# Kernel optimization log

Hardware: AMD Instinct MI355X
Metric: run time of the kernel (lower is better)

## Reference

```python
import jax, jax.numpy as jnp
import numpy as np

B, T, C, UNITS = 64, 1000, 320, 320


def _lstm_scan(x_tbc, m_tb, W, U, b):
    """Masked LSTM over leading time axis.
    x_tbc: [T,B,C], m_tb: [T,B] bool. Keras gate order i,f,c(g),o.
    Masked steps carry (h,c) through unchanged and emit the carried h,
    matching Keras masking semantics. Returns (ys [T,B,U], h_T [B,U]).
    """
    units = U.shape[0]
    h0 = jnp.zeros((x_tbc.shape[1], units), x_tbc.dtype)

    def step(carry, inp):
        h, c = carry
        xt, mt = inp
        z = xt @ W + h @ U + b                      # [B, 4U]
        i, f, g, o = jnp.split(z, 4, axis=-1)
        i = jax.nn.sigmoid(i)
        f = jax.nn.sigmoid(f)
        g = jnp.tanh(g)
        o = jax.nn.sigmoid(o)
        c_new = f * c + i * g
        h_new = o * jnp.tanh(c_new)
        mt = mt[:, None]
        h = jnp.where(mt, h_new, h)
        c = jnp.where(mt, c_new, c)
        return (h, c), h

    (hT, cT), ys = jax.lax.scan(step, (h0, h0), (x_tbc, m_tb))
    return ys, hT


def setup_inputs() -> dict:
    key = jax.random.key(0)
    ks = jax.random.split(key, 8)
    inputs = jax.random.normal(ks[0], (B, T, C), dtype=jnp.float32)
    # padding mask: variable sequence lengths in [T//2, T]
    seq_len = jax.random.randint(ks[1], (B,), T // 2, T + 1)
    mask = (jnp.arange(T)[None, :] < seq_len[:, None])  # [B, T] bool
    s_in = 1.0 / np.sqrt(C)
    s_rec = 1.0 / np.sqrt(UNITS)
    W_fwd = jax.random.normal(ks[2], (C, 4 * UNITS), jnp.float32) * s_in
    U_fwd = jax.random.normal(ks[3], (UNITS, 4 * UNITS), jnp.float32) * s_rec
    b_fwd = jnp.zeros((4 * UNITS,), jnp.float32).at[UNITS:2 * UNITS].set(1.0)  # unit forget bias
    W_bwd = jax.random.normal(ks[4], (C, 4 * UNITS), jnp.float32) * s_in
    U_bwd = jax.random.normal(ks[5], (UNITS, 4 * UNITS), jnp.float32) * s_rec
    b_bwd = jnp.zeros((4 * UNITS,), jnp.float32).at[UNITS:2 * UNITS].set(1.0)
    return {"inputs": inputs, "mask": mask, "W_fwd": W_fwd, "U_fwd": U_fwd,
            "b_fwd": b_fwd, "W_bwd": W_bwd, "U_bwd": U_bwd, "b_bwd": b_bwd}


def reference(inputs, mask, W_fwd, U_fwd, b_fwd, W_bwd, U_bwd, b_bwd):
    x = jnp.transpose(inputs, (1, 0, 2))   # [T,B,C]
    m = jnp.transpose(mask, (1, 0))        # [T,B]
    # forward direction
    ys_f, h_f = _lstm_scan(x, m, W_fwd, U_fwd, b_fwd)
    # backward direction: go_backwards reverses time; Bidirectional flips output back
    ys_b, h_b = _lstm_scan(x[::-1], m[::-1], W_bwd, U_bwd, b_bwd)
    ys_b = ys_b[::-1]
    sequence_output = jnp.transpose(jnp.concatenate([ys_f, ys_b], axis=-1), (1, 0, 2))  # [B,T,2U]
    state_output = jnp.concatenate([h_f, h_b], axis=-1)  # [B,2U]
    return sequence_output, state_output
```

## Files before the change

### kernel.cpp

```cpp
#include <hip/hip_runtime.h>
#include <hip/hip_bf16.h>
#include <stdint.h>


#define Bx 64
#define Tx 1000
#define Cx 320
#define NSLICE 20
#define UPW 16
#define SENT 0xFFFFFFFFFFFFFFFFull

typedef __attribute__((ext_vector_type(8))) short short8;
typedef __attribute__((ext_vector_type(4))) short short4v;
typedef __attribute__((ext_vector_type(4))) float f32x4;

__device__ inline unsigned short f2bf(float f) {
  unsigned x = __builtin_bit_cast(unsigned, f);
  x += 0x7fffu + ((x >> 16) & 1u);
  return (unsigned short)(x >> 16);
}
__device__ inline float bf2f(unsigned short u) {
  unsigned x = ((unsigned)u) << 16;
  return __builtin_bit_cast(float, x);
}

#define OFF_MB   0ull
#define OFF_HB   16384ull
#define OFF_XB   0ull
#define OFF_WT   40960000ull
#define OFF_BP   42598400ull
#define OFF_ZX   42608640ull

__global__ __launch_bounds__(256) void k_prep_x(const float* __restrict__ X,
                                                unsigned short* __restrict__ Xb) {
  int i4 = blockIdx.x * 256 + threadIdx.x;
  if (i4 >= Bx * Tx * Cx / 4) return;
  int idx = i4 * 4;
  int b = idx / (Tx * Cx);
  int rem = idx - b * (Tx * Cx);
  int t = rem / Cx;
  int c = rem - t * Cx;
  float4 v = *(const float4*)(X + idx);
  short4v o;
  o[0] = (short)f2bf(v.x); o[1] = (short)f2bf(v.y);
  o[2] = (short)f2bf(v.z); o[3] = (short)f2bf(v.w);
  *(short4v*)(Xb + (size_t)(t * Bx + b) * Cx + c) = o;
}

__global__ __launch_bounds__(256) void k_prep_w(const float* __restrict__ Wf,
                                                const float* __restrict__ Wb,
                                                const float* __restrict__ bfv,
                                                const float* __restrict__ bbv,
                                                unsigned short* __restrict__ Wt,
                                                float* __restrict__ biasp) {
  int gid = blockIdx.x * 256 + threadIdx.x;
  if (gid < 2 * 1280 * 320) {
    int dir = gid / (1280 * 320);
    int rem = gid - dir * 1280 * 320;
    int n = rem / 320;
    int k = rem - n * 320;
    const float* W = dir ? Wb : Wf;
    Wt[gid] = f2bf(W[k * 1280 + n]);
  }
  if (gid < 2 * 1280) {
    int dir = gid / 1280, n = gid - dir * 1280;
    const float* bsrc = dir ? bbv : bfv;
    biasp[gid] = bsrc[n];
  }
}

__global__ __launch_bounds__(256) void k_prep_mask(const void* __restrict__ maskp,
                                                   unsigned long long* __restrict__ mask2) {
  int t = blockIdx.x * 256 + threadIdx.x;
  if (t >= Tx) return;
  const unsigned* mw = (const unsigned*)maskp;
  const bool mbyte = (mw[0] == 0x01010101u);
  unsigned long long wv = 0ull;
  if (mbyte) {
    const unsigned char* m8 = (const unsigned char*)maskp;
#pragma unroll 8
    for (int b = 0; b < Bx; b++)
      wv |= (unsigned long long)(m8[b * Tx + t] & 1) << b;
  } else {
    const int* m32 = (const int*)maskp;
#pragma unroll 8
    for (int b = 0; b < Bx; b++)
      wv |= (unsigned long long)(m32[b * Tx + t] & 1) << b;
  }
  mask2[t] = wv;
}

__global__ __launch_bounds__(256) void k_gemm(const unsigned short* __restrict__ A,
                                              const unsigned short* __restrict__ Bt,
                                              const float* __restrict__ biasp,
                                              unsigned short* __restrict__ Czx) {
  int bid = blockIdx.x;
  int dir = bid / 5000;
  int r = bid - dir * 5000;
  int tm = r / 10, tn = r - (r / 10) * 10;
  long m0 = (long)tm * 128;
  int n0 = tn * 128;
  const unsigned short* Bd = Bt + (size_t)dir * 1280 * 320;
  const float* bias = biasp + dir * 1280;

  __shared__ __align__(16) unsigned short As[128 * 64];
  __shared__ __align__(16) unsigned short Bs[128 * 64];

  int tid = threadIdx.x;
  int wave = tid >> 6, lane = tid & 63;
  int l15 = lane & 15, l4 = lane >> 4;

  f32x4 acc[2][8];
#pragma unroll
  for (int i = 0; i < 2; i++)
#pragma unroll
    for (int j = 0; j < 8; j++) acc[i][j] = (f32x4){0.f, 0.f, 0.f, 0.f};

  for (int k0 = 0; k0 < 320; k0 += 64) {
    __syncthreads();
#pragma unroll
    for (int it = 0; it < 4; it++) {
      int idx = it * 256 + tid;
      int rr = idx >> 3, cc = idx & 7;
      const unsigned short* ga = A + (size_t)(m0 + rr) * 320 + k0 + cc * 8;
      unsigned short* la = As + (size_t)(it * 256 + wave * 64) * 8;
      __builtin_amdgcn_global_load_lds(
          (const __attribute__((address_space(1))) void*)ga,
          (__attribute__((address_space(3))) void*)la, 16, 0, 0);
      const unsigned short* gb = Bd + (size_t)(n0 + rr) * 320 + k0 + cc * 8;
      unsigned short* lb = Bs + (size_t)(it * 256 + wave * 64) * 8;
      __builtin_amdgcn_global_load_lds(
          (const __attribute__((address_space(1))) void*)gb,
          (__attribute__((address_space(3))) void*)lb, 16, 0, 0);
    }
    __syncthreads();
#pragma unroll
    for (int kk = 0; kk < 2; kk++) {
      short8 af[2], bf8[8];
#pragma unroll
      for (int mf = 0; mf < 2; mf++)
        af[mf] = *(const short8*)(As + (wave * 32 + mf * 16 + l15) * 64 + kk * 32 + l4 * 8);
#pragma unroll
      for (int nf = 0; nf < 8; nf++)
        bf8[nf] = *(const short8*)(Bs + (nf * 16 + l15) * 64 + kk * 32 + l4 * 8);
#pragma unroll
      for (int mf = 0; mf < 2; mf++)
#pragma unroll
        for (int nf = 0; nf < 8; nf++)
          acc[mf][nf] = __builtin_amdgcn_mfma_f32_16x16x32_bf16(af[mf], bf8[nf], acc[mf][nf], 0, 0, 0);
    }
  }
#pragma unroll
  for (int mf = 0; mf < 2; mf++) {
#pragma unroll
    for (int nf = 0; nf < 8; nf++) {
      int col = n0 + nf * 16 + l15;
      float bv = bias[col];
      int g = col / 320;
      int u = col - g * 320;
      int sl = u >> 4;
      int cp = g * 16 + (u & 15);
      size_t sbase = ((size_t)(dir * NSLICE + sl)) * Tx * 4096;
#pragma unroll
      for (int i = 0; i < 4; i++) {
        long m = m0 + wave * 32 + mf * 16 + l4 * 4 + i;
        long t = m >> 6;
        int b = (int)(m & 63);
        Czx[sbase + (size_t)t * 4096 + b * 64 + cp] = f2bf(acc[mf][nf][i] + bv);
      }
    }
  }
}

__global__ __launch_bounds__(256, 1) void k_lstm(const unsigned short* __restrict__ Zx,
                                                 const float* __restrict__ Uf,
                                                 const float* __restrict__ Ub,
                                                 const unsigned long long* __restrict__ mask2,
                                                 unsigned short* __restrict__ hring,
                                                 float* __restrict__ out) {
  const int w = blockIdx.x;
  const int dir = w / NSLICE;
  const int slice = w - dir * NSLICE;
  const int u0 = slice * UPW;
  const int tid = threadIdx.x;
  const int wave = tid >> 6, lane = tid & 63;
  const int l15 = lane & 15, q4 = lane >> 4;

  const float* U = dir ? Ub : Uf;
  short8 bfrag[4][10];
#pragma unroll
  for (int g = 0; g < 4; g++) {
    int colU = g * 320 + u0 + l15;
#pragma unroll
    for (int kt = 0; kt < 10; kt++) {
      short8 v;
#pragma unroll
      for (int j = 0; j < 8; j++)
        v[j] = (short)f2bf(U[(size_t)(kt * 32 + q4 * 8 + j) * 1280 + colU]);
      bfrag[g][kt] = v;
    }
  }

  const int b = 16 * wave + l15;
  float cst0 = 0.f, cst1 = 0.f, cst2 = 0.f, cst3 = 0.f;
  float hst0 = 0.f, hst1 = 0.f, hst2 = 0.f, hst3 = 0.f;

  const unsigned short* zbase = Zx + ((size_t)(dir * NSLICE + slice)) * Tx * 4096;
#define HR(SL) (hring + ((size_t)((SL) * 2 + dir)) * Bx * 320)

  int t = dir ? (Tx - 1) : 0;
  unsigned long long zx0 = *(const unsigned long long*)(zbase + (size_t)t * 4096 + b * 64 + 0 * 16 + 4 * q4);
  unsigned long long zx1 = *(const unsigned long long*)(zbase + (size_t)t * 4096 + b * 64 + 1 * 16 + 4 * q4);
  unsigned long long zx2 = *(const unsigned long long*)(zbase + (size_t)t * 4096 + b * 64 + 2 * 16 + 4 * q4);
  unsigned long long zx3 = *(const unsigned long long*)(zbase + (size_t)t * 4096 + b * 64 + 3 * 16 + 4 * q4);
  unsigned long long mwrd = mask2[t];

  unsigned long long q[20];
  const unsigned short* pollb = nullptr;

  for (int s = 0;; ++s) {
    t = dir ? (Tx - 1 - s) : s;
    f32x4 acc0 = {0.f, 0.f, 0.f, 0.f}, acc1 = {0.f, 0.f, 0.f, 0.f};
    f32x4 acc2 = {0.f, 0.f, 0.f, 0.f}, acc3 = {0.f, 0.f, 0.f, 0.f};
    if (s > 0) {
      unsigned spin = 0;
      for (;;) {
        bool any = false;
#pragma unroll
        for (int i = 0; i < 20; i++) any |= (q[i] == SENT);
        if (!any) break;
        if (++spin > 65536u) break;
#pragma unroll
        for (int i = 0; i < 20; i++)
          if (q[i] == SENT)
            q[i] = __hip_atomic_load(
                (const unsigned long long*)(pollb + (i >> 1) * 32 + q4 * 8 + (i & 1) * 4),
                __ATOMIC_RELAXED, __HIP_MEMORY_SCOPE_AGENT);
      }
      short8 afr[10];
#pragma unroll
      for (int kt = 0; kt < 10; kt++) {
        union { unsigned long long qq[2]; short8 v; } u;
        u.qq[0] = q[2 * kt];
        u.qq[1] = q[2 * kt + 1];
        afr[kt] = u.v;
      }
#pragma unroll
      for (int k2 = 0; k2 < 5; k2++) {
        acc0 = __builtin_amdgcn_mfma_f32_16x16x32_bf16(bfrag[0][2 * k2], afr[2 * k2], acc0, 0, 0, 0);
        acc1 = __builtin_amdgcn_mfma_f32_16x16x32_bf16(bfrag[1][2 * k2], afr[2 * k2], acc1, 0, 0, 0);
        acc2 = __builtin_amdgcn_mfma_f32_16x16x32_bf16(bfrag[2][2 * k2], afr[2 * k2], acc2, 0, 0, 0);
        acc3 = __builtin_amdgcn_mfma_f32_16x16x32_bf16(bfrag[3][2 * k2], afr[2 * k2], acc3, 0, 0, 0);
        acc0 = __builtin_amdgcn_mfma_f32_16x16x32_bf16(bfrag[0][2 * k2 + 1], afr[2 * k2 + 1], acc0, 0, 0, 0);
        acc1 = __builtin_amdgcn_mfma_f32_16x16x32_bf16(bfrag[1][2 * k2 + 1], afr[2 * k2 + 1], acc1, 0, 0, 0);
        acc2 = __builtin_amdgcn_mfma_f32_16x16x32_bf16(bfrag[2][2 * k2 + 1], afr[2 * k2 + 1], acc2, 0, 0, 0);
        acc3 = __builtin_amdgcn_mfma_f32_16x16x32_bf16(bfrag[3][2 * k2 + 1], afr[2 * k2 + 1], acc3, 0, 0, 0);
      }
    }

    int mv = (int)((mwrd >> b) & 1ull);
#define GATES(R, CC, HH)                                               \
    {                                                                  \
      float zi = acc0[R] + bf2f((unsigned short)(zx0 >> (16 * R)));    \
      float zf = acc1[R] + bf2f((unsigned short)(zx1 >> (16 * R)));    \
      float zg = acc2[R] + bf2f((unsigned short)(zx2 >> (16 * R)));    \
      float zo = acc3[R] + bf2f((unsigned short)(zx3 >> (16 * R)));    \
      float ig = 1.f / (1.f + __expf(-zi));                            \
      float fg = 1.f / (1.f + __expf(-zf));                            \
      float gg = 2.f / (1.f + __expf(-2.f * zg)) - 1.f;                \
      float og = 1.f / (1.f + __expf(-zo));                            \
      float cn = fg * (CC) + ig * gg;                                  \
      float hn = og * (2.f / (1.f + __expf(-2.f * cn)) - 1.f);         \
      if (mv) { (CC) = cn; (HH) = hn; }                                \
    }
    GATES(0, cst0, hst0)
    GATES(1, cst1, hst1)
    GATES(2, cst2, hst2)
    GATES(3, cst3, hst3)
#undef GATES

    asm volatile("s_waitcnt vmcnt(0)" ::: "memory");

    if (s < Tx - 1) {
      unsigned long long hv =
          (unsigned long long)f2bf(hst0) | ((unsigned long long)f2bf(hst1) << 16) |
          ((unsigned long long)f2bf(hst2) << 32) | ((unsigned long long)f2bf(hst3) << 48);
      __hip_atomic_store((unsigned long long*)(HR(s & 3) + b * 320 + u0 + 4 * q4),
                         hv, __ATOMIC_RELAXED, __HIP_MEMORY_SCOPE_AGENT);
    }

    float4 ov = make_float4(hst0, hst1, hst2, hst3);
    *(float4*)(out + ((size_t)b * Tx + t) * 640 + dir * 320 + u0 + 4 * q4) = ov;
    if (s == Tx - 1) {
      *(float4*)(out + 40960000ull + (size_t)b * 640 + dir * 320 + u0 + 4 * q4) = ov;
      break;
    }

    __hip_atomic_store((unsigned long long*)(HR((s + 2) & 3) + b * 320 + u0 + 4 * q4),
                       SENT, __ATOMIC_RELAXED, __HIP_MEMORY_SCOPE_AGENT);

    int tn = dir ? (Tx - 2 - s) : (s + 1);
    zx0 = *(const unsigned long long*)(zbase + (size_t)tn * 4096 + b * 64 + 0 * 16 + 4 * q4);
    zx1 = *(const unsigned long long*)(zbase + (size_t)tn * 4096 + b * 64 + 1 * 16 + 4 * q4);
    zx2 = *(const unsigned long long*)(zbase + (size_t)tn * 4096 + b * 64 + 2 * 16 + 4 * q4);
    zx3 = *(const unsigned long long*)(zbase + (size_t)tn * 4096 + b * 64 + 3 * 16 + 4 * q4);
    mwrd = mask2[tn];

    pollb = HR(s & 3) + b * 320;
#pragma unroll
    for (int i = 0; i < 20; i++)
      q[i] = __hip_atomic_load(
          (const unsigned long long*)(pollb + (i >> 1) * 32 + q4 * 8 + (i & 1) * 4),
          __ATOMIC_RELAXED, __HIP_MEMORY_SCOPE_AGENT);
  }
#undef HR
}

extern "C" void kernel_launch(void* const* d_in, const int* in_sizes, int n_in,
                              void* d_out, int out_size, void* d_ws, size_t ws_size,
                              hipStream_t stream) {
  const float* X = (const float*)d_in[0];
  const void* Mk = d_in[1];
  const float* Wf = (const float*)d_in[2];
  const float* Uf = (const float*)d_in[3];
  const float* bfv = (const float*)d_in[4];
  const float* Wb = (const float*)d_in[5];
  const float* Ub = (const float*)d_in[6];
  const float* bbv = (const float*)d_in[7];

  char* ws = (char*)d_ws;
  unsigned short* Xb = (unsigned short*)(ws + OFF_XB);
  unsigned short* Wt = (unsigned short*)(ws + OFF_WT);
  float* bp = (float*)(ws + OFF_BP);
  unsigned short* Zx = (unsigned short*)(ws + OFF_ZX);
  unsigned long long* mask2 = (unsigned long long*)(ws + OFF_MB);
  unsigned short* hring = (unsigned short*)(ws + OFF_HB);

  k_prep_x<<<dim3(20000), dim3(256), 0, stream>>>(X, Xb);
  k_prep_w<<<dim3(3200), dim3(256), 0, stream>>>(Wf, Wb, bfv, bbv, Wt, bp);
  k_gemm<<<dim3(10000), dim3(256), 0, stream>>>(Xb, Wt, bp, Zx);
  hipMemsetAsync(ws + OFF_HB, 0xFF, 327680, stream);
  k_prep_mask<<<dim3(4), dim3(256), 0, stream>>>(Mk, mask2);
  k_lstm<<<dim3(2 * NSLICE), dim3(256), 0, stream>>>(Zx, Uf, Ub, mask2, hring,
                                                     (float*)d_out);
}
```

Baseline: 5.385 ms.

## Halve LSTM workgroups by giving each 512-thread block 32 hidden units

The recurrent kernel now runs 10 slices per direction, each with 8 waves covering 32 units, instead of 20 slices of 4 waves covering 16 units. The Zx layout from the GEMM epilogue is changed to match. This reduces the number of blocks taking part in the per-step cross-block h exchange, which may cut polling and synchronisation overhead. The h-ring stores also switch from relaxed atomic stores to atomicExch, which is an RMW and may cost more per store.

```diff
diff --git a/kernel.cpp b/kernel.cpp
--- a/kernel.cpp
+++ b/kernel.cpp
@@ -6,8 +6,8 @@
 #define Bx 64
 #define Tx 1000
 #define Cx 320
-#define NSLICE 20
-#define UPW 16
+#define NSLICE 10
+#define UPW 32
 #define SENT 0xFFFFFFFFFFFFFFFFull
 
 typedef __attribute__((ext_vector_type(8))) short short8;
@@ -158,21 +158,21 @@
       float bv = bias[col];
       int g = col / 320;
       int u = col - g * 320;
-      int sl = u >> 4;
-      int cp = g * 16 + (u & 15);
-      size_t sbase = ((size_t)(dir * NSLICE + sl)) * Tx * 4096;
+      int sl = u >> 5;
+      int cp = g * 32 + (u & 31);
+      size_t sbase = ((size_t)(dir * NSLICE + sl)) * Tx * 8192;
 #pragma unroll
       for (int i = 0; i < 4; i++) {
         long m = m0 + wave * 32 + mf * 16 + l4 * 4 + i;
         long t = m >> 6;
         int b = (int)(m & 63);
-        Czx[sbase + (size_t)t * 4096 + b * 64 + cp] = f2bf(acc[mf][nf][i] + bv);
+        Czx[sbase + (size_t)t * 8192 + b * 128 + cp] = f2bf(acc[mf][nf][i] + bv);
       }
     }
   }
 }
 
-__global__ __launch_bounds__(256, 1) void k_lstm(const unsigned short* __restrict__ Zx,
+__global__ __launch_bounds__(512, 1) void k_lstm(const unsigned short* __restrict__ Zx,
                                                  const float* __restrict__ Uf,
                                                  const float* __restrict__ Ub,
                                                  const unsigned long long* __restrict__ mask2,
@@ -185,12 +185,14 @@
   const int tid = threadIdx.x;
   const int wave = tid >> 6, lane = tid & 63;
   const int l15 = lane & 15, q4 = lane >> 4;
+  const int hh = wave >> 2;
+  const int ub = u0 + 16 * hh;
 
   const float* U = dir ? Ub : Uf;
   short8 bfrag[4][10];
 #pragma unroll
   for (int g = 0; g < 4; g++) {
-    int colU = g * 320 + u0 + l15;
+    int colU = g * 320 + ub + l15;
 #pragma unroll
     for (int kt = 0; kt < 10; kt++) {
       short8 v;
@@ -201,18 +203,19 @@
     }
   }
 
-  const int b = 16 * wave + l15;
+  const int b = 16 * (wave & 3) + l15;
   float cst0 = 0.f, cst1 = 0.f, cst2 = 0.f, cst3 = 0.f;
   float hst0 = 0.f, hst1 = 0.f, hst2 = 0.f, hst3 = 0.f;
 
-  const unsigned short* zbase = Zx + ((size_t)(dir * NSLICE + slice)) * Tx * 4096;
+  const unsigned short* zbase = Zx + ((size_t)(dir * NSLICE + slice)) * Tx * 8192;
 #define HR(SL) (hring + ((size_t)((SL) * 2 + dir)) * Bx * 320)
 
   int t = dir ? (Tx - 1) : 0;
-  unsigned long long zx0 = *(const unsigned long long*)(zbase + (size_t)t * 4096 + b * 64 + 0 * 16 + 4 * q4);
-  unsigned long long zx1 = *(const unsigned long long*)(zbase + (size_t)t * 4096 + b * 64 + 1 * 16 + 4 * q4);
-  unsigned long long zx2 = *(const unsigned long long*)(zbase + (size_t)t * 4096 + b * 64 + 2 * 16 + 4 * q4);
-  unsigned long long zx3 = *(const unsigned long long*)(zbase + (size_t)t * 4096 + b * 64 + 3 * 16 + 4 * q4);
+  const int zoff = 16 * hh + 4 * q4;
+  unsigned long long zx0 = *(const unsigned long long*)(zbase + (size_t)t * 8192 + b * 128 + 0 * 32 + zoff);
+  unsigned long long zx1 = *(const unsigned long long*)(zbase + (size_t)t * 8192 + b * 128 + 1 * 32 + zoff);
+  unsigned long long zx2 = *(const unsigned long long*)(zbase + (size_t)t * 8192 + b * 128 + 2 * 32 + zoff);
+  unsigned long long zx3 = *(const unsigned long long*)(zbase + (size_t)t * 8192 + b * 128 + 3 * 32 + zoff);
   unsigned long long mwrd = mask2[t];
 
   unsigned long long q[20];
@@ -285,25 +288,23 @@
       unsigned long long hv =
           (unsigned long long)f2bf(hst0) | ((unsigned long long)f2bf(hst1) << 16) |
           ((unsigned long long)f2bf(hst2) << 32) | ((unsigned long long)f2bf(hst3) << 48);
-      __hip_atomic_store((unsigned long long*)(HR(s & 3) + b * 320 + u0 + 4 * q4),
-                         hv, __ATOMIC_RELAXED, __HIP_MEMORY_SCOPE_AGENT);
+      atomicExch((unsigned long long*)(HR(s & 3) + b * 320 + ub + 4 * q4), hv);
     }
 
     float4 ov = make_float4(hst0, hst1, hst2, hst3);
-    *(float4*)(out + ((size_t)b * Tx + t) * 640 + dir * 320 + u0 + 4 * q4) = ov;
+    *(float4*)(out + ((size_t)b * Tx + t) * 640 + dir * 320 + ub + 4 * q4) = ov;
     if (s == Tx - 1) {
-      *(float4*)(out + 40960000ull + (size_t)b * 640 + dir * 320 + u0 + 4 * q4) = ov;
+      *(float4*)(out + 40960000ull + (size_t)b * 640 + dir * 320 + ub + 4 * q4) = ov;
       break;
     }
 
-    __hip_atomic_store((unsigned long long*)(HR((s + 2) & 3) + b * 320 + u0 + 4 * q4),
-                       SENT, __ATOMIC_RELAXED, __HIP_MEMORY_SCOPE_AGENT);
+    atomicExch((unsigned long long*)(HR((s + 2) & 3) + b * 320 + ub + 4 * q4), SENT);
 
     int tn = dir ? (Tx - 2 - s) : (s + 1);
-    zx0 = *(const unsigned long long*)(zbase + (size_t)tn * 4096 + b * 64 + 0 * 16 + 4 * q4);
-    zx1 = *(const unsigned long long*)(zbase + (size_t)tn * 4096 + b * 64 + 1 * 16 + 4 * q4);
-    zx2 = *(const unsigned long long*)(zbase + (size_t)tn * 4096 + b * 64 + 2 * 16 + 4 * q4);
-    zx3 = *(const unsigned long long*)(zbase + (size_t)tn * 4096 + b * 64 + 3 * 16 + 4 * q4);
+    zx0 = *(const unsigned long long*)(zbase + (size_t)tn * 8192 + b * 128 + 0 * 32 + zoff);
+    zx1 = *(const unsigned long long*)(zbase + (size_t)tn * 8192 + b * 128 + 1 * 32 + zoff);
+    zx2 = *(const unsigned long long*)(zbase + (size_t)tn * 8192 + b * 128 + 2 * 32 + zoff);
+    zx3 = *(const unsigned long long*)(zbase + (size_t)tn * 8192 + b * 128 + 3 * 32 + zoff);
     mwrd = mask2[tn];
 
     pollb = HR(s & 3) + b * 320;
@@ -341,6 +342,6 @@
   k_gemm<<<dim3(10000), dim3(256), 0, stream>>>(Xb, Wt, bp, Zx);
   hipMemsetAsync(ws + OFF_HB, 0xFF, 327680, stream);
   k_prep_mask<<<dim3(4), dim3(256), 0, stream>>>(Mk, mask2);
-  k_lstm<<<dim3(2 * NSLICE), dim3(256), 0, stream>>>(Zx, Uf, Ub, mask2, hring,
+  k_lstm<<<dim3(2 * NSLICE), dim3(512), 0, stream>>>(Zx, Uf, Ub, mask2, hring,
                                                      (float*)d_out);
 }
```

New measurement: 10.46 ms. +94.2%, slower.

## Replace shared hidden-state ring with per-consumer mailboxes and consumer-side reset

Applied to the files above, without the earlier changes.

Each LSTM block now broadcasts its bf16 hidden-state slice into a private mailbox for every consumer block in the same direction, instead of writing once to a shared 4-slot ring. Each consumer clears its own previous slot with sentinels instead of the producer clearing the shared slot. Polling loads for the next step are issued right after the producer store. The aim is to cut cross-block contention and coherence traffic on shared lines in the per-timestep handoff. In exchange, each lane issues 20x more stores per step and the mailbox memset grows to several MB.

```diff
diff --git a/kernel.cpp b/kernel.cpp
--- a/kernel.cpp
+++ b/kernel.cpp
@@ -9,6 +9,8 @@
 #define NSLICE 20
 #define UPW 16
 #define SENT 0xFFFFFFFFFFFFFFFFull
+#define SLOT_E (Bx * 320)
+#define CONS_E (4 * SLOT_E)
 
 typedef __attribute__((ext_vector_type(8))) short short8;
 typedef __attribute__((ext_vector_type(4))) short short4v;
@@ -25,7 +27,7 @@
 }
 
 #define OFF_MB   0ull
-#define OFF_HB   16384ull
+#define OFF_MBX  65536ull
 #define OFF_XB   0ull
 #define OFF_WT   40960000ull
 #define OFF_BP   42598400ull
@@ -176,7 +178,7 @@
                                                  const float* __restrict__ Uf,
                                                  const float* __restrict__ Ub,
                                                  const unsigned long long* __restrict__ mask2,
-                                                 unsigned short* __restrict__ hring,
+                                                 unsigned short* __restrict__ mbox,
                                                  float* __restrict__ out) {
   const int w = blockIdx.x;
   const int dir = w / NSLICE;
@@ -206,7 +208,10 @@
   float hst0 = 0.f, hst1 = 0.f, hst2 = 0.f, hst3 = 0.f;
 
   const unsigned short* zbase = Zx + ((size_t)(dir * NSLICE + slice)) * Tx * 4096;
-#define HR(SL) (hring + ((size_t)((SL) * 2 + dir)) * Bx * 320)
+  unsigned short* mydir = mbox + (size_t)dir * NSLICE * CONS_E;
+  unsigned short* mybox = mydir + (size_t)slice * CONS_E;
+  const size_t prod_off = (size_t)b * 320 + u0 + 4 * q4;
+  const size_t poll_off = (size_t)b * 320;
 
   int t = dir ? (Tx - 1) : 0;
   unsigned long long zx0 = *(const unsigned long long*)(zbase + (size_t)t * 4096 + b * 64 + 0 * 16 + 4 * q4);
@@ -285,8 +290,18 @@
       unsigned long long hv =
           (unsigned long long)f2bf(hst0) | ((unsigned long long)f2bf(hst1) << 16) |
           ((unsigned long long)f2bf(hst2) << 32) | ((unsigned long long)f2bf(hst3) << 48);
-      __hip_atomic_store((unsigned long long*)(HR(s & 3) + b * 320 + u0 + 4 * q4),
-                         hv, __ATOMIC_RELAXED, __HIP_MEMORY_SCOPE_AGENT);
+      unsigned short* mp = mydir + (size_t)(s & 3) * SLOT_E + prod_off;
+#pragma unroll
+      for (int c = 0; c < NSLICE; c++)
+        __hip_atomic_store((unsigned long long*)(mp + (size_t)c * CONS_E), hv,
+                           __ATOMIC_RELAXED, __HIP_MEMORY_SCOPE_AGENT);
+
+      pollb = mybox + (size_t)(s & 3) * SLOT_E + poll_off;
+#pragma unroll
+      for (int i = 0; i < 20; i++)
+        q[i] = __hip_atomic_load(
+            (const unsigned long long*)(pollb + (i >> 1) * 32 + q4 * 8 + (i & 1) * 4),
+            __ATOMIC_RELAXED, __HIP_MEMORY_SCOPE_AGENT);
     }
 
     float4 ov = make_float4(hst0, hst1, hst2, hst3);
@@ -296,8 +311,14 @@
       break;
     }
 
-    __hip_atomic_store((unsigned long long*)(HR((s + 2) & 3) + b * 320 + u0 + 4 * q4),
-                       SENT, __ATOMIC_RELAXED, __HIP_MEMORY_SCOPE_AGENT);
+    if (s > 0) {
+      unsigned short* rb = mybox + (size_t)((s - 1) & 3) * SLOT_E + poll_off;
+#pragma unroll
+      for (int i = 0; i < 20; i++)
+        __hip_atomic_store(
+            (unsigned long long*)(rb + (i >> 1) * 32 + q4 * 8 + (i & 1) * 4), SENT,
+            __ATOMIC_RELAXED, __HIP_MEMORY_SCOPE_AGENT);
+    }
 
     int tn = dir ? (Tx - 2 - s) : (s + 1);
     zx0 = *(const unsigned long long*)(zbase + (size_t)tn * 4096 + b * 64 + 0 * 16 + 4 * q4);
@@ -305,15 +326,7 @@
     zx2 = *(const unsigned long long*)(zbase + (size_t)tn * 4096 + b * 64 + 2 * 16 + 4 * q4);
     zx3 = *(const unsigned long long*)(zbase + (size_t)tn * 4096 + b * 64 + 3 * 16 + 4 * q4);
     mwrd = mask2[tn];
-
-    pollb = HR(s & 3) + b * 320;
-#pragma unroll
-    for (int i = 0; i < 20; i++)
-      q[i] = __hip_atomic_load(
-          (const unsigned long long*)(pollb + (i >> 1) * 32 + q4 * 8 + (i & 1) * 4),
-          __ATOMIC_RELAXED, __HIP_MEMORY_SCOPE_AGENT);
-  }
-#undef HR
+  }
 }
 
 extern "C" void kernel_launch(void* const* d_in, const int* in_sizes, int n_in,
@@ -334,13 +347,13 @@
   float* bp = (float*)(ws + OFF_BP);
   unsigned short* Zx = (unsigned short*)(ws + OFF_ZX);
   unsigned long long* mask2 = (unsigned long long*)(ws + OFF_MB);
-  unsigned short* hring = (unsigned short*)(ws + OFF_HB);
+  unsigned short* mbox = (unsigned short*)(ws + OFF_MBX);
 
   k_prep_x<<<dim3(20000), dim3(256), 0, stream>>>(X, Xb);
   k_prep_w<<<dim3(3200), dim3(256), 0, stream>>>(Wf, Wb, bfv, bbv, Wt, bp);
   k_gemm<<<dim3(10000), dim3(256), 0, stream>>>(Xb, Wt, bp, Zx);
-  hipMemsetAsync(ws + OFF_HB, 0xFF, 327680, stream);
+  hipMemsetAsync(ws + OFF_MBX, 0xFF, 6553600, stream);
   k_prep_mask<<<dim3(4), dim3(256), 0, stream>>>(Mk, mask2);
-  k_lstm<<<dim3(2 * NSLICE), dim3(256), 0, stream>>>(Zx, Uf, Ub, mask2, hring,
+  k_lstm<<<dim3(2 * NSLICE), dim3(256), 0, stream>>>(Zx, Uf, Ub, mask2, mbox,
                                                      (float*)d_out);
 }
```

Result: slower. 8.844 ms (+64.2%).

## Poll h ring with coalesced contiguous loads and reshuffle through LDS

Applied to the files above, without the earlier changes.

Each wave now polls its 16 batch rows of the hidden-state ring as one contiguous 10KB block, with lane-contiguous 8-byte atomic loads, instead of strided per-lane reads. The data is then scattered into a padded LDS buffer and read back as MFMA A fragments. Sentinel checks switch to wave-wide ballots per row group, and the poll is issued right after the h store instead of after the next Zx prefetch. The goal is better coalescing on the latency-critical cross-block exchange, at the cost of an LDS round trip and an lgkmcnt wait each step.

```diff
diff --git a/kernel.cpp b/kernel.cpp
--- a/kernel.cpp
+++ b/kernel.cpp
@@ -13,6 +13,7 @@
 typedef __attribute__((ext_vector_type(8))) short short8;
 typedef __attribute__((ext_vector_type(4))) short short4v;
 typedef __attribute__((ext_vector_type(4))) float f32x4;
+typedef __attribute__((ext_vector_type(2))) unsigned long long u64x2;
 
 __device__ inline unsigned short f2bf(float f) {
   unsigned x = __builtin_bit_cast(unsigned, f);
@@ -186,6 +187,16 @@
   const int wave = tid >> 6, lane = tid & 63;
   const int l15 = lane & 15, q4 = lane >> 4;
 
+  __shared__ __align__(16) unsigned char hlds[4][16 * 656];
+  unsigned char* myl = &hlds[wave][0];
+
+  int lofs[10];
+#pragma unroll
+  for (int r = 0; r < 10; r++) {
+    int ci = r * 64 + lane;
+    lofs[r] = (ci / 40) * 656 + (ci % 40) * 16;
+  }
+
   const float* U = dir ? Ub : Uf;
   short8 bfrag[4][10];
 #pragma unroll
@@ -215,8 +226,8 @@
   unsigned long long zx3 = *(const unsigned long long*)(zbase + (size_t)t * 4096 + b * 64 + 3 * 16 + 4 * q4);
   unsigned long long mwrd = mask2[t];
 
-  unsigned long long q[20];
-  const unsigned short* pollb = nullptr;
+  u64x2 pv[10];
+  const unsigned char* pwb = nullptr;
 
   for (int s = 0;; ++s) {
     t = dir ? (Tx - 1 - s) : s;
@@ -225,26 +236,34 @@
     if (s > 0) {
       unsigned spin = 0;
       for (;;) {
-        bool any = false;
-#pragma unroll
-        for (int i = 0; i < 20; i++) any |= (q[i] == SENT);
-        if (!any) break;
+        unsigned pmask = 0;
+#pragma unroll
+        for (int r = 0; r < 10; r++)
+          if (__ballot(pv[r][0] == SENT || pv[r][1] == SENT)) pmask |= 1u << r;
+        if (!pmask) break;
         if (++spin > 65536u) break;
 #pragma unroll
-        for (int i = 0; i < 20; i++)
-          if (q[i] == SENT)
-            q[i] = __hip_atomic_load(
-                (const unsigned long long*)(pollb + (i >> 1) * 32 + q4 * 8 + (i & 1) * 4),
+        for (int r = 0; r < 10; r++)
+          if (pmask & (1u << r)) {
+            pv[r][0] = __hip_atomic_load(
+                (const unsigned long long*)(pwb + r * 1024 + lane * 16),
                 __ATOMIC_RELAXED, __HIP_MEMORY_SCOPE_AGENT);
+            pv[r][1] = __hip_atomic_load(
+                (const unsigned long long*)(pwb + r * 1024 + lane * 16 + 8),
+                __ATOMIC_RELAXED, __HIP_MEMORY_SCOPE_AGENT);
+          }
       }
+#pragma unroll
+      for (int r = 0; r < 10; r++)
+        *(u64x2*)(myl + lofs[r]) = pv[r];
+      asm volatile("s_waitcnt lgkmcnt(0)" ::: "memory");
+      __builtin_amdgcn_sched_barrier(0);
+
       short8 afr[10];
 #pragma unroll
-      for (int kt = 0; kt < 10; kt++) {
-        union { unsigned long long qq[2]; short8 v; } u;
-        u.qq[0] = q[2 * kt];
-        u.qq[1] = q[2 * kt + 1];
-        afr[kt] = u.v;
-      }
+      for (int kt = 0; kt < 10; kt++)
+        afr[kt] = *(const short8*)(myl + l15 * 656 + kt * 64 + q4 * 16);
+
 #pragma unroll
       for (int k2 = 0; k2 < 5; k2++) {
         acc0 = __builtin_amdgcn_mfma_f32_16x16x32_bf16(bfrag[0][2 * k2], afr[2 * k2], acc0, 0, 0, 0);
@@ -287,6 +306,17 @@
           ((unsigned long long)f2bf(hst2) << 32) | ((unsigned long long)f2bf(hst3) << 48);
       __hip_atomic_store((unsigned long long*)(HR(s & 3) + b * 320 + u0 + 4 * q4),
                          hv, __ATOMIC_RELAXED, __HIP_MEMORY_SCOPE_AGENT);
+
+      pwb = (const unsigned char*)(HR(s & 3) + (size_t)(16 * wave) * 320);
+#pragma unroll
+      for (int r = 0; r < 10; r++) {
+        pv[r][0] = __hip_atomic_load(
+            (const unsigned long long*)(pwb + r * 1024 + lane * 16),
+            __ATOMIC_RELAXED, __HIP_MEMORY_SCOPE_AGENT);
+        pv[r][1] = __hip_atomic_load(
+            (const unsigned long long*)(pwb + r * 1024 + lane * 16 + 8),
+            __ATOMIC_RELAXED, __HIP_MEMORY_SCOPE_AGENT);
+      }
     }
 
     float4 ov = make_float4(hst0, hst1, hst2, hst3);
@@ -305,13 +335,6 @@
     zx2 = *(const unsigned long long*)(zbase + (size_t)tn * 4096 + b * 64 + 2 * 16 + 4 * q4);
     zx3 = *(const unsigned long long*)(zbase + (size_t)tn * 4096 + b * 64 + 3 * 16 + 4 * q4);
     mwrd = mask2[tn];
-
-    pollb = HR(s & 3) + b * 320;
-#pragma unroll
-    for (int i = 0; i < 20; i++)
-      q[i] = __hip_atomic_load(
-          (const unsigned long long*)(pollb + (i >> 1) * 32 + q4 * 8 + (i & 1) * 4),
-          __ATOMIC_RELAXED, __HIP_MEMORY_SCOPE_AGENT);
   }
 #undef HR
 }
```

Measured after the change: 5.419 ms. About the same (+0.6%).
